# Kernel tuning notes

Measured on AMD Instinct MI355X. Metric: run time of the kernel, lower is better.

Reference implementation:

```python
import jax, jax.numpy as jnp
import numpy as np

N = 100000
D = 64
E = 1600000
ALPHA = 0.1
BETA = 0.5


def setup_inputs() -> dict:
    key = jax.random.key(0)
    k1, k2, k3, k4, k5, k6 = jax.random.split(key, 6)
    x = jax.random.normal(k1, (N, D), dtype=jnp.float32)
    h0 = jax.random.normal(k2, (N, D), dtype=jnp.float32)
    edge_row = jax.random.randint(k3, (E,), 0, N, dtype=jnp.int32)
    edge_col = jax.random.randint(k4, (E,), 0, N, dtype=jnp.int32)
    edge_val = jax.random.uniform(k5, (E,), dtype=jnp.float32)
    # kaiming_uniform_(a=sqrt(5)) ~= uniform(-1/sqrt(fan_in), 1/sqrt(fan_in)) up to gain; plain normal scaled is fine as a stand-in param
    bound = 1.0 / np.sqrt(D)
    weight = jax.random.uniform(k6, (D, D), dtype=jnp.float32, minval=-bound, maxval=bound)
    return {"x": x, "h0": h0, "edge_row": edge_row, "edge_col": edge_col,
            "edge_val": edge_val, "weight": weight}


def reference(x, h0, edge_row, edge_col, edge_val, weight):
    # support = (1 - alpha) * x + alpha * h0
    support = (1.0 - ALPHA) * x + ALPHA * h0  # [N, D]
    # sparse spmm: out[i] = sum_{e: row[e]==i} val[e] * support[col[e]]
    msgs = edge_val[:, None] * support[edge_col]  # [E, D]
    agg = jax.ops.segment_sum(msgs, edge_row, num_segments=N)  # [N, D]
    # convex blend with dense matmul branch
    out = (1.0 - BETA) * agg + BETA * (support @ weight)  # [N, D]
    return out
```

## Files before the change

### kernel.cpp

```cpp
#include <hip/hip_runtime.h>
#include <hip/hip_bf16.h>

#define DIM 64

__global__ __launch_bounds__(256) void support_dense_kernel(
    const float* __restrict__ x, const float* __restrict__ h0,
    const float* __restrict__ weight,
    __hip_bfloat16* __restrict__ sup_bf,
    float* __restrict__ sup_f32,
    float* __restrict__ out, int n)
{
    __shared__ float s_tile[64][68];
    __shared__ float w_tile[64][68];

    const int tid = threadIdx.x;
    for (int i = tid; i < 64 * 64; i += 256)
        w_tile[i >> 6][i & 63] = weight[i];

    const int row0 = blockIdx.x * 64;

    for (int p = tid; p < 2048; p += 256) {
        const int r = p >> 5;
        const int c = (p & 31) << 1;
        const int row = row0 + r;
        float2 s2;
        if (row < n) {
            const size_t base = (size_t)row * DIM + c;
            const float2 xv = *(const float2*)&x[base];
            const float2 hv = *(const float2*)&h0[base];
            s2.x = 0.9f * xv.x + 0.1f * hv.x;
            s2.y = 0.9f * xv.y + 0.1f * hv.y;
            if (sup_bf) {
                __hip_bfloat162 b2;
                b2.x = __float2bfloat16(s2.x);
                b2.y = __float2bfloat16(s2.y);
                *(__hip_bfloat162*)&sup_bf[base] = b2;
            }
            if (sup_f32) {
                *(float2*)&sup_f32[base] = s2;
            }
        } else {
            s2.x = 0.f; s2.y = 0.f;
        }
        s_tile[r][c] = s2.x;
        s_tile[r][c + 1] = s2.y;
    }
    __syncthreads();

    const int tx = tid & 15, ty = tid >> 4;
    const int r0 = ty * 4, c0 = tx * 4;
    float acc[4][4] = {};
    #pragma unroll
    for (int k = 0; k < 64; k += 4) {
        float4 a[4], b[4];
        #pragma unroll
        for (int i = 0; i < 4; ++i) a[i] = *(const float4*)&s_tile[r0 + i][k];
        #pragma unroll
        for (int j = 0; j < 4; ++j) b[j] = *(const float4*)&w_tile[k + j][c0];
        #pragma unroll
        for (int i = 0; i < 4; ++i) {
            acc[i][0] = fmaf(a[i].x, b[0].x, acc[i][0]);
            acc[i][1] = fmaf(a[i].x, b[0].y, acc[i][1]);
            acc[i][2] = fmaf(a[i].x, b[0].z, acc[i][2]);
            acc[i][3] = fmaf(a[i].x, b[0].w, acc[i][3]);
            acc[i][0] = fmaf(a[i].y, b[1].x, acc[i][0]);
            acc[i][1] = fmaf(a[i].y, b[1].y, acc[i][1]);
            acc[i][2] = fmaf(a[i].y, b[1].z, acc[i][2]);
            acc[i][3] = fmaf(a[i].y, b[1].w, acc[i][3]);
            acc[i][0] = fmaf(a[i].z, b[2].x, acc[i][0]);
            acc[i][1] = fmaf(a[i].z, b[2].y, acc[i][1]);
            acc[i][2] = fmaf(a[i].z, b[2].z, acc[i][2]);
            acc[i][3] = fmaf(a[i].z, b[2].w, acc[i][3]);
            acc[i][0] = fmaf(a[i].w, b[3].x, acc[i][0]);
            acc[i][1] = fmaf(a[i].w, b[3].y, acc[i][1]);
            acc[i][2] = fmaf(a[i].w, b[3].z, acc[i][2]);
            acc[i][3] = fmaf(a[i].w, b[3].w, acc[i][3]);
        }
    }
    #pragma unroll
    for (int i = 0; i < 4; ++i) {
        const int row = row0 + r0 + i;
        if (row < n) {
            float4 o;
            o.x = 0.5f * acc[i][0]; o.y = 0.5f * acc[i][1];
            o.z = 0.5f * acc[i][2]; o.w = 0.5f * acc[i][3];
            *(float4*)&out[(size_t)row * DIM + c0] = o;
        }
    }
}

__global__ __launch_bounds__(256) void hist_kernel(
    const int* __restrict__ erow, int* __restrict__ counts, int e)
{
    int idx = blockIdx.x * blockDim.x + threadIdx.x;
    const int stride = gridDim.x * blockDim.x;
    for (int i = idx; i < e; i += stride)
        atomicAdd(&counts[erow[i]], 1);
}

__global__ __launch_bounds__(256) void scan1_kernel(
    const int* __restrict__ counts, int* __restrict__ ex,
    int* __restrict__ blockSums, int n)
{
    __shared__ int lds[256];
    const int t = threadIdx.x;
    const int base = blockIdx.x * 1024 + t * 4;
    int v[4]; int sum = 0;
    #pragma unroll
    for (int j = 0; j < 4; ++j) {
        const int idx = base + j;
        v[j] = (idx < n) ? counts[idx] : 0;
        sum += v[j];
    }
    lds[t] = sum;
    __syncthreads();
    #pragma unroll
    for (int off = 1; off < 256; off <<= 1) {
        const int y = (t >= off) ? lds[t - off] : 0;
        __syncthreads();
        lds[t] += y;
        __syncthreads();
    }
    const int excl_t = lds[t] - sum;
    if (t == 255) blockSums[blockIdx.x] = lds[255];
    int run = excl_t;
    #pragma unroll
    for (int j = 0; j < 4; ++j) {
        const int idx = base + j;
        if (idx < n) ex[idx] = run;
        run += v[j];
    }
}

__global__ __launch_bounds__(128) void scan2_kernel(int* __restrict__ bs, int nb)
{
    __shared__ int lds[128];
    const int t = threadIdx.x;
    const int v = (t < nb) ? bs[t] : 0;
    lds[t] = v;
    __syncthreads();
    #pragma unroll
    for (int off = 1; off < 128; off <<= 1) {
        const int y = (t >= off) ? lds[t - off] : 0;
        __syncthreads();
        lds[t] += y;
        __syncthreads();
    }
    if (t < nb) bs[t] = lds[t] - v;
}

__global__ __launch_bounds__(256) void scan3_kernel(
    int* __restrict__ rowStart, int* __restrict__ cursor,
    const int* __restrict__ blockSums, int n, int e)
{
    const int i = blockIdx.x * blockDim.x + threadIdx.x;
    if (i < n) {
        const int v = rowStart[i] + blockSums[i >> 10];
        rowStart[i] = v;
        cursor[i] = v;
    }
    if (i == 0) rowStart[n] = e;
}

__global__ __launch_bounds__(256) void scatter_part_kernel(
    const int* __restrict__ erow, const int* __restrict__ ecol,
    const float* __restrict__ eval_, int* __restrict__ cursor,
    int2* __restrict__ cv, int e, int rlo_chunk)
{
    const int part = blockIdx.x & 7;
    const int bip  = blockIdx.x >> 3;
    const int nbp  = gridDim.x >> 3;
    const int rlo = part * rlo_chunk;
    const int rhi = rlo + rlo_chunk;

    int idx = bip * blockDim.x + threadIdx.x;
    const int stride = nbp * blockDim.x;
    for (int i = idx; i < e; i += stride) {
        const int r = erow[i];
        if (r >= rlo && r < rhi) {
            const int c = ecol[i];
            const float v = eval_[i];
            const int p = atomicAdd(&cursor[r], 1);
            cv[p] = make_int2(c, __float_as_int(v));
        }
    }
}

__global__ __launch_bounds__(256) void aggregate_kernel(
    const int* __restrict__ rowStart, const int2* __restrict__ cv,
    const __hip_bfloat16* __restrict__ sup_bf, float* __restrict__ out, int n)
{
    const int row = blockIdx.x * 4 + (threadIdx.x >> 6);
    if (row >= n) return;
    const int lane = threadIdx.x & 63;
    const int s = rowStart[row], e = rowStart[row + 1];
    float acc = 0.f;
    int i = s;
    for (; i + 4 <= e; i += 4) {
        const int2 c0 = cv[i], c1 = cv[i + 1], c2 = cv[i + 2], c3 = cv[i + 3];
        const float m0 = __bfloat162float(sup_bf[(size_t)c0.x * DIM + lane]);
        const float m1 = __bfloat162float(sup_bf[(size_t)c1.x * DIM + lane]);
        const float m2 = __bfloat162float(sup_bf[(size_t)c2.x * DIM + lane]);
        const float m3 = __bfloat162float(sup_bf[(size_t)c3.x * DIM + lane]);
        acc = fmaf(__int_as_float(c0.y), m0, acc);
        acc = fmaf(__int_as_float(c1.y), m1, acc);
        acc = fmaf(__int_as_float(c2.y), m2, acc);
        acc = fmaf(__int_as_float(c3.y), m3, acc);
    }
    for (; i < e; ++i) {
        const int2 c0 = cv[i];
        acc = fmaf(__int_as_float(c0.y),
                   __bfloat162float(sup_bf[(size_t)c0.x * DIM + lane]), acc);
    }
    const size_t base = (size_t)row * DIM + lane;
    out[base] = fmaf(0.5f, acc, out[base]);
}

__global__ __launch_bounds__(256) void spmm_atomic_kernel(
    const int* __restrict__ erow, const int* __restrict__ ecol,
    const float* __restrict__ eval_, const float* __restrict__ support,
    float* __restrict__ out, int e)
{
    const long total = (long)e * DIM;
    long idx = (long)blockIdx.x * blockDim.x + threadIdx.x;
    const long stride = (long)gridDim.x * blockDim.x;
    for (long t = idx; t < total; t += stride) {
        const int edge = (int)(t >> 6);
        const int j = (int)(t & 63);
        const float m = 0.5f * eval_[edge] * support[(long)ecol[edge] * DIM + j];
        atomicAdd(&out[(long)erow[edge] * DIM + j], m);
    }
}

extern "C" void kernel_launch(void* const* d_in, const int* in_sizes, int n_in,
                              void* d_out, int out_size, void* d_ws, size_t ws_size,
                              hipStream_t stream) {
    const float* x      = (const float*)d_in[0];
    const float* h0     = (const float*)d_in[1];
    const int*   erow   = (const int*)d_in[2];
    const int*   ecol   = (const int*)d_in[3];
    const float* eval_  = (const float*)d_in[4];
    const float* weight = (const float*)d_in[5];
    float* out = (float*)d_out;

    const int n = in_sizes[0] / DIM;
    const int e = in_sizes[2];

    char* wsb = (char*)d_ws;
    size_t off = 0;
    auto alloc = [&](size_t bytes) { size_t o = off; off = (off + bytes + 255) & ~255ULL; return o; };
    const size_t o_supbf = alloc((size_t)n * DIM * 2);
    const size_t o_cv    = alloc((size_t)e * 8);
    const size_t o_rowst = alloc((size_t)(n + 1) * 4);
    const size_t o_curs  = alloc((size_t)n * 4);
    const size_t o_cnts  = alloc((size_t)n * 4);
    const size_t o_bsums = alloc(512);
    const size_t need = off;

    const int nb1 = (n + 1023) / 1024;

    if (ws_size >= need && nb1 <= 128) {
        __hip_bfloat16* sup_bf = (__hip_bfloat16*)(wsb + o_supbf);
        int2* cv      = (int2*)(wsb + o_cv);
        int* rowStart = (int*)(wsb + o_rowst);
        int* cursor   = (int*)(wsb + o_curs);
        int* counts   = (int*)(wsb + o_cnts);
        int* bsums    = (int*)(wsb + o_bsums);

        hipMemsetAsync(counts, 0, (size_t)n * 4, stream);

        support_dense_kernel<<<(n + 63) / 64, 256, 0, stream>>>(
            x, h0, weight, sup_bf, nullptr, out, n);
        hist_kernel<<<2048, 256, 0, stream>>>(erow, counts, e);
        scan1_kernel<<<nb1, 256, 0, stream>>>(counts, rowStart, bsums, n);
        scan2_kernel<<<1, 128, 0, stream>>>(bsums, nb1);
        scan3_kernel<<<(n + 255) / 256, 256, 0, stream>>>(rowStart, cursor, bsums, n, e);

        const int rchunk = (n + 7) / 8;
        scatter_part_kernel<<<4096, 256, 0, stream>>>(erow, ecol, eval_, cursor, cv, e, rchunk);

        aggregate_kernel<<<(n + 3) / 4, 256, 0, stream>>>(rowStart, cv, sup_bf, out, n);
    } else {
        float* support = (float*)d_ws;
        support_dense_kernel<<<(n + 63) / 64, 256, 0, stream>>>(
            x, h0, weight, nullptr, support, out, n);
        spmm_atomic_kernel<<<16384, 256, 0, stream>>>(erow, ecol, eval_, support, out, e);
    }
}
```

Measured before the change: 374.2 us.

## Split support/GEMM kernels, read bf16 support in GEMM, add nontemporal edge loads

The fused support+dense kernel is split into a streaming elementwise kernel that writes bf16 support and a separate GEMM kernel that reads the bf16 support back instead of x and h0. Edge-list and CSR reads in the hist, scatter and aggregate kernels now use nontemporal loads, intended to keep L2 for the gathered support rows. The GEMM k-loop unroll is reduced to 2. The extra launch and the bf16 input to the dense branch add overhead and slightly change numerics, while the GEMM reads half the bytes it did before.

```diff
diff --git a/kernel.cpp b/kernel.cpp
--- a/kernel.cpp
+++ b/kernel.cpp
@@ -3,12 +3,33 @@
 
 #define DIM 64
 
-__global__ __launch_bounds__(256) void support_dense_kernel(
+__device__ __forceinline__ int   nt_i(const int* p)   { return __builtin_nontemporal_load(p); }
+__device__ __forceinline__ float nt_f(const float* p) { return __builtin_nontemporal_load(p); }
+__device__ __forceinline__ long long nt_ll(const void* p) {
+    return __builtin_nontemporal_load((const long long*)p);
+}
+
+__global__ __launch_bounds__(256) void support_bf16_kernel(
     const float* __restrict__ x, const float* __restrict__ h0,
-    const float* __restrict__ weight,
-    __hip_bfloat16* __restrict__ sup_bf,
-    float* __restrict__ sup_f32,
-    float* __restrict__ out, int n)
+    __hip_bfloat16* __restrict__ sup_bf, long total4)
+{
+    long idx = (long)blockIdx.x * blockDim.x + threadIdx.x;
+    const long stride = (long)gridDim.x * blockDim.x;
+    for (long t = idx; t < total4; t += stride) {
+        const float4 xv = ((const float4*)x)[t];
+        const float4 hv = ((const float4*)h0)[t];
+        union { ushort4 u4; __hip_bfloat16 h[4]; } cvt;
+        cvt.h[0] = __float2bfloat16(0.9f * xv.x + 0.1f * hv.x);
+        cvt.h[1] = __float2bfloat16(0.9f * xv.y + 0.1f * hv.y);
+        cvt.h[2] = __float2bfloat16(0.9f * xv.z + 0.1f * hv.z);
+        cvt.h[3] = __float2bfloat16(0.9f * xv.w + 0.1f * hv.w);
+        ((ushort4*)sup_bf)[t] = cvt.u4;
+    }
+}
+
+__global__ __launch_bounds__(256) void dense_gemm_kernel(
+    const __hip_bfloat16* __restrict__ sup_bf,
+    const float* __restrict__ weight, float* __restrict__ out, int n)
 {
     __shared__ float s_tile[64][68];
     __shared__ float w_tile[64][68];
@@ -18,39 +39,28 @@
         w_tile[i >> 6][i & 63] = weight[i];
 
     const int row0 = blockIdx.x * 64;
-
-    for (int p = tid; p < 2048; p += 256) {
-        const int r = p >> 5;
-        const int c = (p & 31) << 1;
+    for (int p = tid; p < 1024; p += 256) {
+        const int r = p >> 4;
+        const int c = (p & 15) << 2;
         const int row = row0 + r;
-        float2 s2;
         if (row < n) {
-            const size_t base = (size_t)row * DIM + c;
-            const float2 xv = *(const float2*)&x[base];
-            const float2 hv = *(const float2*)&h0[base];
-            s2.x = 0.9f * xv.x + 0.1f * hv.x;
-            s2.y = 0.9f * xv.y + 0.1f * hv.y;
-            if (sup_bf) {
-                __hip_bfloat162 b2;
-                b2.x = __float2bfloat16(s2.x);
-                b2.y = __float2bfloat16(s2.y);
-                *(__hip_bfloat162*)&sup_bf[base] = b2;
-            }
-            if (sup_f32) {
-                *(float2*)&sup_f32[base] = s2;
-            }
+            union { ushort4 u4; __hip_bfloat16 h[4]; } cvt;
+            cvt.u4 = *(const ushort4*)&sup_bf[(size_t)row * DIM + c];
+            s_tile[r][c]     = __bfloat162float(cvt.h[0]);
+            s_tile[r][c + 1] = __bfloat162float(cvt.h[1]);
+            s_tile[r][c + 2] = __bfloat162float(cvt.h[2]);
+            s_tile[r][c + 3] = __bfloat162float(cvt.h[3]);
         } else {
-            s2.x = 0.f; s2.y = 0.f;
-        }
-        s_tile[r][c] = s2.x;
-        s_tile[r][c + 1] = s2.y;
+            s_tile[r][c] = 0.f; s_tile[r][c+1] = 0.f;
+            s_tile[r][c+2] = 0.f; s_tile[r][c+3] = 0.f;
+        }
     }
     __syncthreads();
 
     const int tx = tid & 15, ty = tid >> 4;
     const int r0 = ty * 4, c0 = tx * 4;
     float acc[4][4] = {};
-    #pragma unroll
+    #pragma unroll 2
     for (int k = 0; k < 64; k += 4) {
         float4 a[4], b[4];
         #pragma unroll
@@ -95,7 +105,7 @@
     int idx = blockIdx.x * blockDim.x + threadIdx.x;
     const int stride = gridDim.x * blockDim.x;
     for (int i = idx; i < e; i += stride)
-        atomicAdd(&counts[erow[i]], 1);
+        atomicAdd(&counts[nt_i(&erow[i])], 1);
 }
 
 __global__ __launch_bounds__(256) void scan1_kernel(
@@ -176,10 +186,10 @@
     int idx = bip * blockDim.x + threadIdx.x;
     const int stride = nbp * blockDim.x;
     for (int i = idx; i < e; i += stride) {
-        const int r = erow[i];
+        const int r = nt_i(&erow[i]);
         if (r >= rlo && r < rhi) {
-            const int c = ecol[i];
-            const float v = eval_[i];
+            const int c = nt_i(&ecol[i]);
+            const float v = nt_f(&eval_[i]);
             const int p = atomicAdd(&cursor[r], 1);
             cv[p] = make_int2(c, __float_as_int(v));
         }
@@ -197,23 +207,105 @@
     float acc = 0.f;
     int i = s;
     for (; i + 4 <= e; i += 4) {
-        const int2 c0 = cv[i], c1 = cv[i + 1], c2 = cv[i + 2], c3 = cv[i + 3];
-        const float m0 = __bfloat162float(sup_bf[(size_t)c0.x * DIM + lane]);
-        const float m1 = __bfloat162float(sup_bf[(size_t)c1.x * DIM + lane]);
-        const float m2 = __bfloat162float(sup_bf[(size_t)c2.x * DIM + lane]);
-        const float m3 = __bfloat162float(sup_bf[(size_t)c3.x * DIM + lane]);
-        acc = fmaf(__int_as_float(c0.y), m0, acc);
-        acc = fmaf(__int_as_float(c1.y), m1, acc);
-        acc = fmaf(__int_as_float(c2.y), m2, acc);
-        acc = fmaf(__int_as_float(c3.y), m3, acc);
+        const long long q0 = nt_ll(&cv[i]);
+        const long long q1 = nt_ll(&cv[i + 1]);
+        const long long q2 = nt_ll(&cv[i + 2]);
+        const long long q3 = nt_ll(&cv[i + 3]);
+        const float m0 = __bfloat162float(sup_bf[(size_t)(int)q0 * DIM + lane]);
+        const float m1 = __bfloat162float(sup_bf[(size_t)(int)q1 * DIM + lane]);
+        const float m2 = __bfloat162float(sup_bf[(size_t)(int)q2 * DIM + lane]);
+        const float m3 = __bfloat162float(sup_bf[(size_t)(int)q3 * DIM + lane]);
+        acc = fmaf(__int_as_float((int)(q0 >> 32)), m0, acc);
+        acc = fmaf(__int_as_float((int)(q1 >> 32)), m1, acc);
+        acc = fmaf(__int_as_float((int)(q2 >> 32)), m2, acc);
+        acc = fmaf(__int_as_float((int)(q3 >> 32)), m3, acc);
     }
     for (; i < e; ++i) {
-        const int2 c0 = cv[i];
-        acc = fmaf(__int_as_float(c0.y),
-                   __bfloat162float(sup_bf[(size_t)c0.x * DIM + lane]), acc);
+        const long long q0 = nt_ll(&cv[i]);
+        acc = fmaf(__int_as_float((int)(q0 >> 32)),
+                   __bfloat162float(sup_bf[(size_t)(int)q0 * DIM + lane]), acc);
     }
     const size_t base = (size_t)row * DIM + lane;
     out[base] = fmaf(0.5f, acc, out[base]);
+}
+
+__global__ __launch_bounds__(256) void support_f32_kernel(
+    const float* __restrict__ x, const float* __restrict__ h0,
+    float* __restrict__ sup, long total4)
+{
+    long idx = (long)blockIdx.x * blockDim.x + threadIdx.x;
+    const long stride = (long)gridDim.x * blockDim.x;
+    for (long t = idx; t < total4; t += stride) {
+        const float4 xv = ((const float4*)x)[t];
+        const float4 hv = ((const float4*)h0)[t];
+        float4 s;
+        s.x = 0.9f * xv.x + 0.1f * hv.x;
+        s.y = 0.9f * xv.y + 0.1f * hv.y;
+        s.z = 0.9f * xv.z + 0.1f * hv.z;
+        s.w = 0.9f * xv.w + 0.1f * hv.w;
+        ((float4*)sup)[t] = s;
+    }
+}
+
+__global__ __launch_bounds__(256) void dense_gemm_f32_kernel(
+    const float* __restrict__ sup, const float* __restrict__ weight,
+    float* __restrict__ out, int n)
+{
+    __shared__ float s_tile[64][68];
+    __shared__ float w_tile[64][68];
+    const int tid = threadIdx.x;
+    for (int i = tid; i < 64 * 64; i += 256)
+        w_tile[i >> 6][i & 63] = weight[i];
+    const int row0 = blockIdx.x * 64;
+    for (int p = tid; p < 2048; p += 256) {
+        const int r = p >> 5;
+        const int c = (p & 31) << 1;
+        const int row = row0 + r;
+        float2 s2 = make_float2(0.f, 0.f);
+        if (row < n) s2 = *(const float2*)&sup[(size_t)row * DIM + c];
+        s_tile[r][c] = s2.x; s_tile[r][c + 1] = s2.y;
+    }
+    __syncthreads();
+    const int tx = tid & 15, ty = tid >> 4;
+    const int r0 = ty * 4, c0 = tx * 4;
+    float acc[4][4] = {};
+    #pragma unroll 2
+    for (int k = 0; k < 64; k += 4) {
+        float4 a[4], b[4];
+        #pragma unroll
+        for (int i = 0; i < 4; ++i) a[i] = *(const float4*)&s_tile[r0 + i][k];
+        #pragma unroll
+        for (int j = 0; j < 4; ++j) b[j] = *(const float4*)&w_tile[k + j][c0];
+        #pragma unroll
+        for (int i = 0; i < 4; ++i) {
+            acc[i][0] = fmaf(a[i].x, b[0].x, acc[i][0]);
+            acc[i][1] = fmaf(a[i].x, b[0].y, acc[i][1]);
+            acc[i][2] = fmaf(a[i].x, b[0].z, acc[i][2]);
+            acc[i][3] = fmaf(a[i].x, b[0].w, acc[i][3]);
+            acc[i][0] = fmaf(a[i].y, b[1].x, acc[i][0]);
+            acc[i][1] = fmaf(a[i].y, b[1].y, acc[i][1]);
+            acc[i][2] = fmaf(a[i].y, b[1].z, acc[i][2]);
+            acc[i][3] = fmaf(a[i].y, b[1].w, acc[i][3]);
+            acc[i][0] = fmaf(a[i].z, b[2].x, acc[i][0]);
+            acc[i][1] = fmaf(a[i].z, b[2].y, acc[i][1]);
+            acc[i][2] = fmaf(a[i].z, b[2].z, acc[i][2]);
+            acc[i][3] = fmaf(a[i].z, b[2].w, acc[i][3]);
+            acc[i][0] = fmaf(a[i].w, b[3].x, acc[i][0]);
+            acc[i][1] = fmaf(a[i].w, b[3].y, acc[i][1]);
+            acc[i][2] = fmaf(a[i].w, b[3].z, acc[i][2]);
+            acc[i][3] = fmaf(a[i].w, b[3].w, acc[i][3]);
+        }
+    }
+    #pragma unroll
+    for (int i = 0; i < 4; ++i) {
+        const int row = row0 + r0 + i;
+        if (row < n) {
+            float4 o;
+            o.x = 0.5f * acc[i][0]; o.y = 0.5f * acc[i][1];
+            o.z = 0.5f * acc[i][2]; o.w = 0.5f * acc[i][3];
+            *(float4*)&out[(size_t)row * DIM + c0] = o;
+        }
+    }
 }
 
 __global__ __launch_bounds__(256) void spmm_atomic_kernel(
@@ -258,6 +350,7 @@
     const size_t need = off;
 
     const int nb1 = (n + 1023) / 1024;
+    const long total4 = (long)n * DIM / 4;
 
     if (ws_size >= need && nb1 <= 128) {
         __hip_bfloat16* sup_bf = (__hip_bfloat16*)(wsb + o_supbf);
@@ -269,21 +362,22 @@
 
         hipMemsetAsync(counts, 0, (size_t)n * 4, stream);
 
-        support_dense_kernel<<<(n + 63) / 64, 256, 0, stream>>>(
-            x, h0, weight, sup_bf, nullptr, out, n);
+        support_bf16_kernel<<<2048, 256, 0, stream>>>(x, h0, sup_bf, total4);
         hist_kernel<<<2048, 256, 0, stream>>>(erow, counts, e);
         scan1_kernel<<<nb1, 256, 0, stream>>>(counts, rowStart, bsums, n);
         scan2_kernel<<<1, 128, 0, stream>>>(bsums, nb1);
         scan3_kernel<<<(n + 255) / 256, 256, 0, stream>>>(rowStart, cursor, bsums, n, e);
 
+        dense_gemm_kernel<<<(n + 63) / 64, 256, 0, stream>>>(sup_bf, weight, out, n);
+
         const int rchunk = (n + 7) / 8;
         scatter_part_kernel<<<4096, 256, 0, stream>>>(erow, ecol, eval_, cursor, cv, e, rchunk);
 
         aggregate_kernel<<<(n + 3) / 4, 256, 0, stream>>>(rowStart, cv, sup_bf, out, n);
     } else {
         float* support = (float*)d_ws;
-        support_dense_kernel<<<(n + 63) / 64, 256, 0, stream>>>(
-            x, h0, weight, nullptr, support, out, n);
+        support_f32_kernel<<<2048, 256, 0, stream>>>(x, h0, support, total4);
+        dense_gemm_f32_kernel<<<(n + 63) / 64, 256, 0, stream>>>(support, weight, out, n);
         spmm_atomic_kernel<<<16384, 256, 0, stream>>>(erow, ecol, eval_, support, out, e);
     }
 }
```

New measurement: 358.9 us. -4.1%, faster.
